# Kernel optimization log

Hardware: AMD Instinct MI355X
Metric: run time of the kernel (lower is better)

Reference implementation:

```python
import jax, jax.numpy as jnp
import numpy as np

R, N, C, E, H, NC = 25, 256, 64, 128, 8, 27


def _layernorm(x, w, b, axes, eps):
    m = x.mean(axis=axes, keepdims=True)
    v = x.var(axis=axes, keepdims=True)
    return (x - m) / jnp.sqrt(v + eps) * w + b


def _mha(emb_ln, idx, WQ, WK):
    # emb_ln: (R*N, E); idx: (L,) district indices
    ew = emb_ln.reshape(R, N, E)[idx]                       # (L,N,E) gather of district blocks
    Q = jnp.einsum('lne,hfe->lhnf', ew, WQ)                 # torch Linear: x @ W.T
    K = jnp.einsum('lne,hfe->lhnf', ew, WK)
    QK = jnp.einsum('lhnf,lhmf->lhnm', Q, K) / jnp.sqrt(jnp.float32(E))
    return jax.nn.softmax(QK, axis=2)                       # torch softmax(dim=1) over (L,n,n)


def setup_inputs() -> dict:
    key = jax.random.key(0)
    ks = jax.random.split(key, 16)
    inp = {
        'business_structure_target': jax.random.normal(ks[0], (R, C, N, 4), jnp.float32),
        'business_structure_infected': jax.random.normal(ks[1], (R, C, N, 4), jnp.float32),
        'customer_structure_target': jax.random.normal(ks[2], (R, C, N, NC, 4), jnp.float32),
        'customer_structure_infected': jax.random.normal(ks[3], (R, C, N, NC, 4), jnp.float32),
        'index_target_idx': jax.random.randint(ks[4], (R, C), 0, R),
        'index_infected_idx': jax.random.randint(ks[5], (R, C), 0, R),
        'covid_outbreak_business': jax.random.randint(ks[6], (R, C), 0, N),
        'emb_table': jax.random.normal(ks[7], (R * N, E), jnp.float32),
        'ln_emb_w': jnp.ones((E,), jnp.float32),
        'ln_emb_b': jnp.zeros((E,), jnp.float32),
        'WQ_trg': jax.random.normal(ks[8], (H, E, E), jnp.float32) * 0.05,
        'WK_trg': jax.random.normal(ks[9], (H, E, E), jnp.float32) * 0.05,
        'WQ_inf': jax.random.normal(ks[10], (H, E, E), jnp.float32) * 0.05,
        'WK_inf': jax.random.normal(ks[11], (H, E, E), jnp.float32) * 0.05,
        'W_os': jax.random.normal(ks[12], (E, E), jnp.float32) * 0.05,
        'b_os': jnp.zeros((E,), jnp.float32),
        'bs_w': jnp.ones((C, N), jnp.float32), 'bs_b': jnp.zeros((C, N), jnp.float32),
        'cs_w': jnp.ones((C, N), jnp.float32), 'cs_b': jnp.zeros((C, N), jnp.float32),
        'os_w': jnp.ones((C, N), jnp.float32), 'os_b': jnp.zeros((C, N), jnp.float32),
    }
    return inp


def reference(business_structure_target, business_structure_infected,
              customer_structure_target, customer_structure_infected,
              index_target_idx, index_infected_idx, covid_outbreak_business,
              emb_table, ln_emb_w, ln_emb_b,
              WQ_trg, WK_trg, WQ_inf, WK_inf,
              W_os, b_os, bs_w, bs_b, cs_w, cs_b, os_w, os_b):
    # mean over feature dim, then slicing per original forward
    bst = business_structure_target.mean(-1)[:R, 0]        # (R,N)
    bsi = business_structure_infected.mean(-1)[0]          # (C,N)
    cst = customer_structure_target.mean(-1)[:R, 0]        # (R,N,NC)
    csi = customer_structure_infected.mean(-1)[0]          # (C,N,NC)

    emb_ln = _layernorm(emb_table, ln_emb_w, ln_emb_b, -1, 1e-16)
    idx_t = index_target_idx[:R, 0]                        # (R,)
    idx_i = index_infected_idx[0]                          # (C,)

    attn_t = _mha(emb_ln, idx_t, WQ_trg, WK_trg)           # (R,H,N,N)
    BR_t = jnp.einsum('ln,lhnm->lmh', bst, attn_t)         # (R,N,H)
    attn_i = _mha(emb_ln, idx_i, WQ_inf, WK_inf)           # (C,H,N,N)
    BR_i = jnp.einsum('cn,chnm->cmh', bsi, attn_i)         # (C,N,H)

    # cosine similarity over head dim, broadcast (R,1,N,H) x (1,C,N,H)
    a = BR_t[:, None]
    b = BR_i[None]
    dot = jnp.sum(a * b, -1)
    na = jnp.linalg.norm(a, axis=-1)
    nb = jnp.linalg.norm(b, axis=-1)
    BS = dot / jnp.maximum(na * nb, 1e-15)                 # (R,C,N)

    # Jensen-Shannon-style KLD over consumer dim (log_target=True semantics)
    log_p = jax.nn.log_softmax(cst, -1)[:, None]           # (R,1,N,NC)
    log_q = jax.nn.log_softmax(csi, -1)[None]              # (1,C,N,NC)
    log_m = jax.nn.log_softmax((log_p + log_q) / 2, -1)
    kl_p = (jnp.exp(log_m) * (log_m - log_p)).mean(-1)
    kl_q = (jnp.exp(log_m) * (log_m - log_q)).mean(-1)
    CS = -(kl_p + kl_q) / 2                                # (R,C,N)

    biz = covid_outbreak_business[0]                       # (C,)
    inf_emb = emb_table[idx_i * N + biz]                   # (C,E) raw (non-LN) embedding
    proj = inf_emb @ W_os.T + b_os
    OS = (proj @ emb_table.T).reshape(C, R, N).transpose(1, 0, 2)  # (R,C,N)

    BS = _layernorm(BS, bs_w, bs_b, (-2, -1), 1e-5)
    CS = _layernorm(CS, cs_w, cs_b, (-2, -1), 1e-5)
    OS = _layernorm(OS, os_w, os_b, (-2, -1), 1e-5)
    return BS, CS, OS
```

## Files before the change

### kernel.cpp

```cpp
#include <hip/hip_runtime.h>
#include <math.h>

#define R_ 25
#define N_ 256
#define C_ 64
#define E_ 128
#define H_ 8
#define NC_ 27
#define SQS 28

typedef _Float16 f16x8 __attribute__((ext_vector_type(8)));
typedef float f32x16 __attribute__((ext_vector_type(16)));

union HU { ushort s; _Float16 h; };
__device__ __forceinline__ ushort ftoh(float f) { HU u; u.h = (_Float16)f; return u.s; }
__device__ __forceinline__ float htof(ushort s) { HU u; u.s = s; return (float)u.h; }

__device__ __forceinline__ float waveReduceSum(float v) {
  #pragma unroll
  for (int off = 32; off > 0; off >>= 1) v += __shfl_xor(v, off);
  return v;
}

__global__ __launch_bounds__(256) void k_prep(
    const float* __restrict__ emb, const float* __restrict__ ln_w,
    const float* __restrict__ ln_b, ushort* __restrict__ emb16,
    const float* __restrict__ bus_t, const float* __restrict__ bus_i,
    float* __restrict__ bst, float* __restrict__ bsi,
    const float* __restrict__ cus_t, const float* __restrict__ cus_i,
    float* __restrict__ Ssq, float* __restrict__ Tsq,
    const int* __restrict__ idx_t, const int* __restrict__ idx_i,
    int* __restrict__ cnt, int* __restrict__ lst,
    const int* __restrict__ biz, const float* __restrict__ Wos,
    const float* __restrict__ bos, float* __restrict__ projb,
    const float* __restrict__ WQt_, const float* __restrict__ WKt_,
    const float* __restrict__ WQi_, const float* __restrict__ WKi_,
    ushort* __restrict__ Gt) {
  __shared__ uint sbuf[16384];
  int bid = blockIdx.x, t = threadIdx.x;
  if (bid < 1600) {
    int row = bid * 4 + (t >> 6);
    int lane = t & 63;
    const float2* x = (const float2*)(emb + (size_t)row * E_);
    float2 v = x[lane];
    float s = waveReduceSum(v.x + v.y);
    float m = s * (1.0f / 128.0f);
    float d0 = v.x - m, d1 = v.y - m;
    float ss = waveReduceSum(d0 * d0 + d1 * d1);
    float inv = 1.0f / sqrtf(ss * (1.0f / 128.0f) + 1e-16f);
    float2 wv = ((const float2*)ln_w)[lane];
    float2 bv = ((const float2*)ln_b)[lane];
    uint u = (uint)ftoh(d0 * inv * wv.x + bv.x) | ((uint)ftoh(d1 * inv * wv.y + bv.y) << 16);
    ((uint*)emb16)[(size_t)row * 64 + lane] = u;
  } else if (bid < 1689) {
    int i = (bid - 1600) * 256 + t;
    if (i < R_ * N_) {
      size_t row = (size_t)(i >> 8) * (C_ * N_) + (i & 255);
      float4 v = *(const float4*)&bus_t[row * 4];
      bst[i] = (v.x + v.y + v.z + v.w) * 0.25f;
    }
    int j = i - R_ * N_;
    if (j >= 0 && j < C_ * N_) {
      float4 v = *(const float4*)&bus_i[(size_t)j * 4];
      bsi[j] = (v.x + v.y + v.z + v.w) * 0.25f;
    }
  } else if (bid < 2045) {
    int gidx = (bid - 1689) * 256 + t;
    int rowi = gidx >> 2, sub = gidx & 3;
    const float* src; float* dst; size_t base; int oi;
    if (rowi < R_ * N_) {
      src = cus_t; dst = Ssq; oi = rowi;
      base = ((size_t)(rowi >> 8) * (C_ * N_) + (rowi & 255)) * (NC_ * 4);
    } else {
      int j = rowi - R_ * N_;
      if (j >= C_ * N_) return;
      src = cus_i; dst = Tsq; oi = j;
      base = ((size_t)(j >> 8) * N_ + (j & 255)) * (NC_ * 4);
    }
    int j0 = sub * 7;
    int nj = (sub == 3) ? 6 : 7;
    float v[7];
    float mx = -1e30f;
    #pragma unroll
    for (int k = 0; k < 7; ++k) {
      if (k < nj) {
        float4 q = *(const float4*)&src[base + (j0 + k) * 4];
        v[k] = (q.x + q.y + q.z + q.w) * 0.25f;
        mx = fmaxf(mx, v[k]);
      }
    }
    mx = fmaxf(mx, __shfl_xor(mx, 1));
    mx = fmaxf(mx, __shfl_xor(mx, 2));
    float se = 0.0f;
    #pragma unroll
    for (int k = 0; k < 7; ++k) if (k < nj) se += expf(v[k] - mx);
    se += __shfl_xor(se, 1);
    se += __shfl_xor(se, 2);
    float lse = mx + logf(se);
    #pragma unroll
    for (int k = 0; k < 7; ++k)
      if (k < nj) dst[(size_t)oi * SQS + j0 + k] = expf(0.5f * (v[k] - lse));
    if (sub == 3) dst[(size_t)oi * SQS + NC_] = 0.0f;
  } else if (bid == 2045) {
    if (t < 2 * R_) cnt[t] = 0;
    __syncthreads();
    if (t < R_) {
      int rr = idx_t[t * C_];
      int pos = atomicAdd(&cnt[rr], 1);
      lst[rr * 64 + pos] = t;
    }
    if (t < C_) {
      int rr = idx_i[t];
      int pos = atomicAdd(&cnt[R_ + rr], 1);
      lst[(R_ + rr) * 64 + pos] = t;
    }
  } else if (bid < 2078) {
    float* er2 = (float*)sbuf;
    int pb = bid - 2046;
    int ci = t >> 7, f = t & 127;
    int c = pb * 2 + ci;
    int row = idx_i[c] * N_ + biz[c];
    er2[ci * E_ + f] = emb[(size_t)row * E_ + f];
    __syncthreads();
    float acc = bos[f];
    const float* wr = &Wos[(size_t)f * E_];
    const float* er = &er2[ci * E_];
    for (int e = 0; e < E_; e += 4) {
      float4 w4 = *(const float4*)&wr[e];
      acc += er[e] * w4.x + er[e + 1] * w4.y + er[e + 2] * w4.z + er[e + 3] * w4.w;
    }
    projb[c * E_ + f] = acc;
  } else {
    int gb = bid - 2078;
    int h = gb & 7, set = gb >> 3;
    const float* WQ = (set ? WQi_ : WQt_) + ((size_t)h << 14);
    const float* WK = (set ? WKi_ : WKt_) + ((size_t)h << 14);
    uint* QT = sbuf;
    uint* KT = sbuf + 8192;
    for (int j = t; j < 8192; j += 256) {
      int e = j & 127, f2 = j >> 7;
      int wi = (f2 << 8) + e;
      float q0 = WQ[wi], q1 = WQ[wi + 128];
      float k0 = WK[wi], k1 = WK[wi + 128];
      int idx = (e << 6) + (f2 ^ ((e & 15) << 2));
      QT[idx] = (uint)ftoh(q0) | ((uint)ftoh(q1) << 16);
      KT[idx] = (uint)ftoh(k0) | ((uint)ftoh(k1) << 16);
    }
    __syncthreads();
    int w = t >> 6, l = t & 63, lo = l & 31, hi = l >> 5;
    int m0 = w << 5;
    f32x16 acc[4];
    #pragma unroll
    for (int i = 0; i < 4; ++i)
      #pragma unroll
      for (int j = 0; j < 16; ++j) acc[i][j] = 0.0f;
    int mrow = m0 + lo;
    #pragma unroll
    for (int ks = 0; ks < 8; ++ks) {
      int f2b = (ks << 3) + (hi << 2);
      f16x8 a = *(const f16x8*)&KT[(mrow << 6) + (f2b ^ ((mrow & 15) << 2))];
      #pragma unroll
      for (int tl = 0; tl < 4; ++tl) {
        int ncol = (tl << 5) + lo;
        f16x8 b = *(const f16x8*)&QT[(ncol << 6) + (f2b ^ ((ncol & 15) << 2))];
        acc[tl] = __builtin_amdgcn_mfma_f32_32x32x16_f16(a, b, acc[tl], 0, 0, 0);
      }
    }
    const float scale = 0.08838834764831845f;
    ushort* Go = Gt + (((size_t)(set * H_ + h)) << 14);
    #pragma unroll
    for (int tl = 0; tl < 4; ++tl)
      #pragma unroll
      for (int rg = 0; rg < 16; ++rg) {
        int row = m0 + (rg & 3) + ((rg >> 2) << 3) + (hi << 2);
        int col = (tl << 5) + lo;
        Go[(row << 7) + col] = ftoh(acc[tl][rg] * scale);
      }
  }
}

__global__ __launch_bounds__(512) void k_attn_fused(
    const ushort* __restrict__ emb16, const ushort* __restrict__ GtAll,
    const int* __restrict__ cnt, const int* __restrict__ lst,
    const float* __restrict__ bst, const float* __restrict__ bsi,
    float* __restrict__ BRt, float* __restrict__ BRi) {
  int r = blockIdx.x, h = blockIdx.y, set = blockIdx.z;
  int g = set * R_ + r;
  int L = cnt[g];
  if (L == 0) return;
  __shared__ ushort ELN[256 * 128];
  __shared__ ushort TA[128 * 128];
  __shared__ ushort TB[128 * 128];
  __shared__ float redA[8 * 128];
  __shared__ float redB[8 * 128];
  __shared__ float gM[128], gD[128];
  int t = threadIdx.x;
  const uint4* Ep = (const uint4*)(emb16 + ((size_t)r << 15));
  for (int c = t; c < 4096; c += 512) {
    int n = c >> 4, s = c & 15;
    uint4 v = Ep[c];
    *(uint4*)&ELN[(n << 7) + ((s << 3) ^ ((n & 15) << 3))] = v;
  }
  const uint4* Gp = (const uint4*)(GtAll + ((size_t)(set * H_ + h) << 14));
  for (int c = t; c < 2048; c += 512) {
    int e2 = c >> 4, s = c & 15;
    uint4 v = Gp[c];
    *(uint4*)&TA[(e2 << 7) + ((s << 3) ^ ((e2 & 15) << 3))] = v;
  }
  __syncthreads();
  int w = t >> 6, l = t & 63, lo = l & 31, hi = l >> 5;
  f32x16 tacc[4];
  #pragma unroll
  for (int i = 0; i < 4; ++i)
    #pragma unroll
    for (int j = 0; j < 16; ++j) tacc[i][j] = 0.0f;
  int n = (w << 5) + lo;
  #pragma unroll
  for (int ks = 0; ks < 8; ++ks) {
    f16x8 a = *(const f16x8*)&ELN[(n << 7) + (((ks << 4) + (hi << 3)) ^ ((n & 15) << 3))];
    #pragma unroll
    for (int tl = 0; tl < 4; ++tl) {
      int f = (tl << 5) + lo;
      f16x8 b = *(const f16x8*)&TA[(f << 7) + (((ks << 4) + (hi << 3)) ^ ((f & 15) << 3))];
      tacc[tl] = __builtin_amdgcn_mfma_f32_32x32x16_f16(a, b, tacc[tl], 0, 0, 0);
    }
  }
  __syncthreads();
  {
    ushort* Tl = (w < 4) ? TA : TB;
    #pragma unroll
    for (int tl = 0; tl < 4; ++tl)
      #pragma unroll
      for (int rg = 0; rg < 16; ++rg) {
        int row = ((w & 3) << 5) + (rg & 3) + ((rg >> 2) << 3) + (hi << 2);
        int col = (tl << 5) + lo;
        Tl[(row << 7) + (col ^ ((row & 15) << 3))] = ftoh(tacc[tl][rg]);
      }
  }
  __syncthreads();
  const float* wv = set ? bsi : bst;
  float* BR = set ? BRi : BRt;
  const ushort* Tl = (w < 4) ? TA : TB;
  int rrow = n & 127;
  int baseRow = (w << 5) + (hi << 2);
  for (int mh = 0; mh < 2; ++mh) {
    f32x16 acc[4];
    #pragma unroll
    for (int i = 0; i < 4; ++i)
      #pragma unroll
      for (int j = 0; j < 16; ++j) acc[i][j] = 0.0f;
    #pragma unroll
    for (int ks = 0; ks < 8; ++ks) {
      f16x8 a = *(const f16x8*)&Tl[(rrow << 7) + (((ks << 4) + (hi << 3)) ^ ((rrow & 15) << 3))];
      #pragma unroll
      for (int tl = 0; tl < 4; ++tl) {
        int m = (mh << 7) + (tl << 5) + lo;
        f16x8 b = *(const f16x8*)&ELN[(m << 7) + (((ks << 4) + (hi << 3)) ^ ((m & 15) << 3))];
        acc[tl] = __builtin_amdgcn_mfma_f32_32x32x16_f16(a, b, acc[tl], 0, 0, 0);
      }
    }
    #pragma unroll
    for (int tl = 0; tl < 4; ++tl) {
      float mx = acc[tl][0];
      #pragma unroll
      for (int rg = 1; rg < 16; ++rg) mx = fmaxf(mx, acc[tl][rg]);
      mx = fmaxf(mx, __shfl_xor(mx, 32));
      if (hi == 0) redA[(w << 7) + (tl << 5) + lo] = mx;
    }
    __syncthreads();
    if (t < 128) {
      float gm = redA[t];
      #pragma unroll
      for (int ww = 1; ww < 8; ++ww) gm = fmaxf(gm, redA[(ww << 7) + t]);
      gM[t] = gm;
    }
    __syncthreads();
    #pragma unroll
    for (int tl = 0; tl < 4; ++tl) {
      float gmv = gM[(tl << 5) + lo];
      float s = 0.0f;
      #pragma unroll
      for (int rg = 0; rg < 16; ++rg) {
        acc[tl][rg] = __expf(acc[tl][rg] - gmv);
        s += acc[tl][rg];
      }
      s += __shfl_xor(s, 32);
      if (hi == 0) redB[(w << 7) + (tl << 5) + lo] = s;
    }
    __syncthreads();
    if (t < 128) {
      float d = 0.0f;
      #pragma unroll
      for (int ww = 0; ww < 8; ++ww) d += redB[(ww << 7) + t];
      gD[t] = d;
    }
    __syncthreads();
    for (int li = 0; li < L; ++li) {
      int ll = lst[g * 64 + li];
      float wreg[16];
      #pragma unroll
      for (int rg = 0; rg < 16; ++rg)
        wreg[rg] = wv[ll * N_ + baseRow + (rg & 3) + ((rg >> 2) << 3)];
      #pragma unroll
      for (int tl = 0; tl < 4; ++tl) {
        float part = 0.0f;
        #pragma unroll
        for (int rg = 0; rg < 16; ++rg) part += wreg[rg] * acc[tl][rg];
        part += __shfl_xor(part, 32);
        if (hi == 0) redA[(w << 7) + (tl << 5) + lo] = part;
      }
      __syncthreads();
      if (t < 128) {
        float s = 0.0f;
        #pragma unroll
        for (int ww = 0; ww < 8; ++ww) s += redA[(ww << 7) + t];
        BR[((size_t)ll * N_ + (mh << 7) + t) * H_ + h] = s / gD[t];
      }
      __syncthreads();
    }
  }
}

__global__ __launch_bounds__(256) void k_bscs_os(
    const float* __restrict__ BRt, const float* __restrict__ BRi,
    const float* __restrict__ Ssq, const float* __restrict__ Tsq,
    const float* __restrict__ emb, const float* __restrict__ projb,
    float* __restrict__ outBS, float* __restrict__ outCS,
    float* __restrict__ outOS,
    float2* __restrict__ pBS, float2* __restrict__ pCS,
    float2* __restrict__ pOS) {
  __shared__ float pr[8][E_];
  __shared__ float rb[4][4];
  int bid = blockIdx.x, t = threadIdx.x;
  if (bid < 1600) {
    int i = bid * 256 + t;
    int n = i & 255, c = (i >> 8) & 63, l = i >> 14;
    const float4* a = (const float4*)&BRt[((size_t)l * N_ + n) * H_];
    const float4* b = (const float4*)&BRi[((size_t)c * N_ + n) * H_];
    float4 a0 = a[0], a1 = a[1], b0 = b[0], b1 = b[1];
    float dot = a0.x * b0.x + a0.y * b0.y + a0.z * b0.z + a0.w * b0.w
              + a1.x * b1.x + a1.y * b1.y + a1.z * b1.z + a1.w * b1.w;
    float na = a0.x * a0.x + a0.y * a0.y + a0.z * a0.z + a0.w * a0.w
             + a1.x * a1.x + a1.y * a1.y + a1.z * a1.z + a1.w * a1.w;
    float nb = b0.x * b0.x + b0.y * b0.y + b0.z * b0.z + b0.w * b0.w
             + b1.x * b1.x + b1.y * b1.y + b1.z * b1.z + b1.w * b1.w;
    float bsv = dot / fmaxf(sqrtf(na) * sqrtf(nb), 1e-15f);
    outBS[i] = bsv;

    const float4* sp = (const float4*)&Ssq[((size_t)l * N_ + n) * SQS];
    const float4* tp = (const float4*)&Tsq[((size_t)c * N_ + n) * SQS];
    float d2 = 0.0f;
    #pragma unroll
    for (int j = 0; j < 7; ++j) {
      float4 sv = sp[j], tv = tp[j];
      d2 += sv.x * tv.x + sv.y * tv.y + sv.z * tv.z + sv.w * tv.w;
    }
    float csv = logf(d2) * (1.0f / 27.0f);
    outCS[i] = csv;
    float s0 = waveReduceSum(bsv), q0 = waveReduceSum(bsv * bsv);
    float s1 = waveReduceSum(csv), q1 = waveReduceSum(csv * csv);
    if ((t & 63) == 0) {
      int wv = t >> 6;
      rb[wv][0] = s0; rb[wv][1] = q0; rb[wv][2] = s1; rb[wv][3] = q1;
    }
    __syncthreads();
    if (t == 0) {
      float A = 0, B = 0, Cq = 0, D = 0;
      #pragma unroll
      for (int k = 0; k < 4; ++k) { A += rb[k][0]; B += rb[k][1]; Cq += rb[k][2]; D += rb[k][3]; }
      pBS[bid] = make_float2(A, B);
      pCS[bid] = make_float2(Cq, D);
    }
  } else {
    int o = bid - 1600;
    int l = o >> 3, cg = o & 7;
    for (int i = t; i < 1024; i += 256)
      pr[i >> 7][i & 127] = projb[(cg * 8 + (i >> 7)) * E_ + (i & 127)];
    __syncthreads();
    const float* er = &emb[((size_t)(l * N_) + t) << 7];
    float acc[8] = {0, 0, 0, 0, 0, 0, 0, 0};
    for (int e = 0; e < 128; e += 4) {
      float4 v = *(const float4*)&er[e];
      #pragma unroll
      for (int c = 0; c < 8; ++c)
        acc[c] += v.x * pr[c][e] + v.y * pr[c][e + 1] + v.z * pr[c][e + 2] + v.w * pr[c][e + 3];
    }
    float s = 0.0f, q = 0.0f;
    #pragma unroll
    for (int c = 0; c < 8; ++c) {
      outOS[((size_t)l * C_ + cg * 8 + c) * N_ + t] = acc[c];
      s += acc[c];
      q += acc[c] * acc[c];
    }
    s = waveReduceSum(s);
    q = waveReduceSum(q);
    if ((t & 63) == 0) { int wv = t >> 6; rb[wv][0] = s; rb[wv][1] = q; }
    __syncthreads();
    if (t == 0) {
      float A = 0, B = 0;
      #pragma unroll
      for (int k = 0; k < 4; ++k) { A += rb[k][0]; B += rb[k][1]; }
      pOS[o] = make_float2(A, B);
    }
  }
}

__global__ __launch_bounds__(256) void k_ln_apply(
    float* __restrict__ out,
    const float2* __restrict__ pBS, const float2* __restrict__ pCS,
    const float2* __restrict__ pOS,
    const float* __restrict__ w0, const float* __restrict__ b0,
    const float* __restrict__ w1, const float* __restrict__ b1,
    const float* __restrict__ w2, const float* __restrict__ b2) {
  int r = blockIdx.x, o = blockIdx.y, chunk = blockIdx.z;
  int t = threadIdx.x;
  __shared__ float sm[2];
  if (t < 64) {
    float s = 0.0f, q = 0.0f;
    if (o == 2) {
      if (t < 8) { float2 v = pOS[r * 8 + t]; s = v.x; q = v.y; }
    } else {
      const float2* pp = (o == 0) ? pBS : pCS;
      float2 v = pp[r * 64 + t]; s = v.x; q = v.y;
    }
    #pragma unroll
    for (int off = 32; off > 0; off >>= 1) {
      s += __shfl_xor(s, off);
      q += __shfl_xor(q, off);
    }
    if (t == 0) {
      float m = s * (1.0f / 16384.0f);
      float v = q * (1.0f / 16384.0f) - m * m;
      sm[0] = m;
      sm[1] = 1.0f / sqrtf(v + 1e-5f);
    }
  }
  __syncthreads();
  float m = sm[0], inv = sm[1];
  const float* w = (o == 0) ? w0 : (o == 1) ? w1 : w2;
  const float* b = (o == 0) ? b0 : (o == 1) ? b1 : b2;
  float* x = out + (size_t)o * 409600 + (size_t)r * 16384;
  int base = chunk * 2048;
  #pragma unroll
  for (int k = 0; k < 8; ++k) {
    int pos = base + k * 256 + t;
    x[pos] = (x[pos] - m) * inv * w[pos] + b[pos];
  }
}

extern "C" void kernel_launch(void* const* d_in, const int* in_sizes, int n_in,
                              void* d_out, int out_size, void* d_ws, size_t ws_size,
                              hipStream_t stream) {
  const float* bus_t  = (const float*)d_in[0];
  const float* bus_i  = (const float*)d_in[1];
  const float* cus_t  = (const float*)d_in[2];
  const float* cus_i  = (const float*)d_in[3];
  const int*   idx_t  = (const int*)d_in[4];
  const int*   idx_i  = (const int*)d_in[5];
  const int*   cov    = (const int*)d_in[6];
  const float* emb    = (const float*)d_in[7];
  const float* ln_w   = (const float*)d_in[8];
  const float* ln_b   = (const float*)d_in[9];
  const float* WQ_trg = (const float*)d_in[10];
  const float* WK_trg = (const float*)d_in[11];
  const float* WQ_inf = (const float*)d_in[12];
  const float* WK_inf = (const float*)d_in[13];
  const float* W_os   = (const float*)d_in[14];
  const float* b_os   = (const float*)d_in[15];
  const float* bs_w   = (const float*)d_in[16];
  const float* bs_b   = (const float*)d_in[17];
  const float* cs_w   = (const float*)d_in[18];
  const float* cs_b   = (const float*)d_in[19];
  const float* os_w   = (const float*)d_in[20];
  const float* os_b   = (const float*)d_in[21];

  float* ws = (float*)d_ws;
  ushort* emb16 = (ushort*)ws;
  float* p = ws + 409600;
  ushort* Gt = (ushort*)p;   p += 131072;
  float* bst = p;            p += 6400;
  float* bsi = p;            p += 16384;
  float* Ssq = p;            p += R_ * N_ * SQS;
  float* Tsq = p;            p += C_ * N_ * SQS;
  float* BRt = p;            p += 51200;
  float* BRi = p;            p += 131072;
  float* projb = p;          p += 8192;
  int* cnt = (int*)p;        p += 64;
  int* lst = (int*)p;        p += 3200;
  float2* pBS = (float2*)p;  p += 3200;
  float2* pCS = (float2*)p;  p += 3200;
  float2* pOS = (float2*)p;  p += 400;

  float* outBS = (float*)d_out;
  float* outCS = outBS + 409600;
  float* outOS = outCS + 409600;

  k_prep<<<2094, 256, 0, stream>>>(emb, ln_w, ln_b, emb16,
                                   bus_t, bus_i, bst, bsi,
                                   cus_t, cus_i, Ssq, Tsq,
                                   idx_t, idx_i, cnt, lst,
                                   cov, W_os, b_os, projb,
                                   WQ_trg, WK_trg, WQ_inf, WK_inf, Gt);
  k_attn_fused<<<dim3(R_, H_, 2), 512, 0, stream>>>(emb16, Gt, cnt, lst,
                                                    bst, bsi, BRt, BRi);
  k_bscs_os<<<1800, 256, 0, stream>>>(BRt, BRi, Ssq, Tsq, emb, projb,
                                      outBS, outCS, outOS, pBS, pCS, pOS);
  k_ln_apply<<<dim3(R_, 3, 8), 256, 0, stream>>>(outBS, pBS, pCS, pOS,
                                                 bs_w, bs_b, cs_w, cs_b, os_w, os_b);
}
```

Before: 84.56 us.

## Read attention operands from global memory and shrink LDS to raise occupancy

```diff
diff --git a/kernel.cpp b/kernel.cpp
--- a/kernel.cpp
+++ b/kernel.cpp
@@ -179,7 +179,7 @@
   }
 }
 
-__global__ __launch_bounds__(512) void k_attn_fused(
+__global__ __launch_bounds__(512, 4) void k_attn_fused(
     const ushort* __restrict__ emb16, const ushort* __restrict__ GtAll,
     const int* __restrict__ cnt, const int* __restrict__ lst,
     const float* __restrict__ bst, const float* __restrict__ bsi,
@@ -188,61 +188,46 @@
   int g = set * R_ + r;
   int L = cnt[g];
   if (L == 0) return;
-  __shared__ ushort ELN[256 * 128];
-  __shared__ ushort TA[128 * 128];
-  __shared__ ushort TB[128 * 128];
+  __shared__ ushort Tbuf[256 * 128];
   __shared__ float redA[8 * 128];
   __shared__ float redB[8 * 128];
   __shared__ float gM[128], gD[128];
   int t = threadIdx.x;
-  const uint4* Ep = (const uint4*)(emb16 + ((size_t)r << 15));
-  for (int c = t; c < 4096; c += 512) {
-    int n = c >> 4, s = c & 15;
-    uint4 v = Ep[c];
-    *(uint4*)&ELN[(n << 7) + ((s << 3) ^ ((n & 15) << 3))] = v;
-  }
-  const uint4* Gp = (const uint4*)(GtAll + ((size_t)(set * H_ + h) << 14));
-  for (int c = t; c < 2048; c += 512) {
-    int e2 = c >> 4, s = c & 15;
-    uint4 v = Gp[c];
-    *(uint4*)&TA[(e2 << 7) + ((s << 3) ^ ((e2 & 15) << 3))] = v;
-  }
-  __syncthreads();
   int w = t >> 6, l = t & 63, lo = l & 31, hi = l >> 5;
+  int n = (w << 5) + lo;
+  const ushort* Ebase = emb16 + ((size_t)r << 15);
+  const ushort* Gp = GtAll + ((size_t)(set * H_ + h) << 14);
+
   f32x16 tacc[4];
   #pragma unroll
   for (int i = 0; i < 4; ++i)
     #pragma unroll
     for (int j = 0; j < 16; ++j) tacc[i][j] = 0.0f;
-  int n = (w << 5) + lo;
+  {
+    const ushort* Ap = Ebase + ((size_t)n << 7) + (hi << 3);
+    #pragma unroll
+    for (int ks = 0; ks < 8; ++ks) {
+      f16x8 a = *(const f16x8*)(Ap + (ks << 4));
+      #pragma unroll
+      for (int tl = 0; tl < 4; ++tl) {
+        int f = (tl << 5) + lo;
+        f16x8 b = *(const f16x8*)(Gp + (f << 7) + (hi << 3) + (ks << 4));
+        tacc[tl] = __builtin_amdgcn_mfma_f32_32x32x16_f16(a, b, tacc[tl], 0, 0, 0);
+      }
+    }
+  }
   #pragma unroll
-  for (int ks = 0; ks < 8; ++ks) {
-    f16x8 a = *(const f16x8*)&ELN[(n << 7) + (((ks << 4) + (hi << 3)) ^ ((n & 15) << 3))];
-    #pragma unroll
-    for (int tl = 0; tl < 4; ++tl) {
-      int f = (tl << 5) + lo;
-      f16x8 b = *(const f16x8*)&TA[(f << 7) + (((ks << 4) + (hi << 3)) ^ ((f & 15) << 3))];
-      tacc[tl] = __builtin_amdgcn_mfma_f32_32x32x16_f16(a, b, tacc[tl], 0, 0, 0);
-    }
-  }
-  __syncthreads();
-  {
-    ushort* Tl = (w < 4) ? TA : TB;
-    #pragma unroll
-    for (int tl = 0; tl < 4; ++tl)
-      #pragma unroll
-      for (int rg = 0; rg < 16; ++rg) {
-        int row = ((w & 3) << 5) + (rg & 3) + ((rg >> 2) << 3) + (hi << 2);
-        int col = (tl << 5) + lo;
-        Tl[(row << 7) + (col ^ ((row & 15) << 3))] = ftoh(tacc[tl][rg]);
-      }
-  }
-  __syncthreads();
+  for (int tl = 0; tl < 4; ++tl)
+    #pragma unroll
+    for (int rg = 0; rg < 16; ++rg) {
+      int row = (w << 5) + (rg & 3) + ((rg >> 2) << 3) + (hi << 2);
+      int col = (tl << 5) + lo;
+      Tbuf[(row << 7) + (col ^ ((row & 15) << 3))] = ftoh(tacc[tl][rg]);
+    }
   const float* wv = set ? bsi : bst;
   float* BR = set ? BRi : BRt;
-  const ushort* Tl = (w < 4) ? TA : TB;
-  int rrow = n & 127;
   int baseRow = (w << 5) + (hi << 2);
+
   for (int mh = 0; mh < 2; ++mh) {
     f32x16 acc[4];
     #pragma unroll
@@ -251,11 +236,11 @@
       for (int j = 0; j < 16; ++j) acc[i][j] = 0.0f;
     #pragma unroll
     for (int ks = 0; ks < 8; ++ks) {
-      f16x8 a = *(const f16x8*)&Tl[(rrow << 7) + (((ks << 4) + (hi << 3)) ^ ((rrow & 15) << 3))];
+      f16x8 a = *(const f16x8*)&Tbuf[(n << 7) + (((ks << 4) + (hi << 3)) ^ ((n & 15) << 3))];
       #pragma unroll
       for (int tl = 0; tl < 4; ++tl) {
         int m = (mh << 7) + (tl << 5) + lo;
-        f16x8 b = *(const f16x8*)&ELN[(m << 7) + (((ks << 4) + (hi << 3)) ^ ((m & 15) << 3))];
+        f16x8 b = *(const f16x8*)(Ebase + ((size_t)m << 7) + (hi << 3) + (ks << 4));
         acc[tl] = __builtin_amdgcn_mfma_f32_32x32x16_f16(a, b, acc[tl], 0, 0, 0);
       }
     }
```

Measured after the change: 105.2 us. +24.4%, slower.

## Transpose attention score tile so softmax and weighted sums stay within each wave

Applied to the files above, without the earlier changes.

```diff
diff --git a/kernel.cpp b/kernel.cpp
--- a/kernel.cpp
+++ b/kernel.cpp
@@ -191,10 +191,9 @@
   __shared__ ushort ELN[256 * 128];
   __shared__ ushort TA[128 * 128];
   __shared__ ushort TB[128 * 128];
-  __shared__ float redA[8 * 128];
-  __shared__ float redB[8 * 128];
-  __shared__ float gM[128], gD[128];
   int t = threadIdx.x;
+  int w = t >> 6, l = t & 63, lo = l & 31, hi = l >> 5;
+
   const uint4* Ep = (const uint4*)(emb16 + ((size_t)r << 15));
   for (int c = t; c < 4096; c += 512) {
     int n = c >> 4, s = c & 15;
@@ -208,25 +207,25 @@
     *(uint4*)&TA[(e2 << 7) + ((s << 3) ^ ((e2 & 15) << 3))] = v;
   }
   __syncthreads();
-  int w = t >> 6, l = t & 63, lo = l & 31, hi = l >> 5;
-  f32x16 tacc[4];
-  #pragma unroll
-  for (int i = 0; i < 4; ++i)
-    #pragma unroll
-    for (int j = 0; j < 16; ++j) tacc[i][j] = 0.0f;
-  int n = (w << 5) + lo;
-  #pragma unroll
-  for (int ks = 0; ks < 8; ++ks) {
-    f16x8 a = *(const f16x8*)&ELN[(n << 7) + (((ks << 4) + (hi << 3)) ^ ((n & 15) << 3))];
-    #pragma unroll
-    for (int tl = 0; tl < 4; ++tl) {
-      int f = (tl << 5) + lo;
-      f16x8 b = *(const f16x8*)&TA[(f << 7) + (((ks << 4) + (hi << 3)) ^ ((f & 15) << 3))];
-      tacc[tl] = __builtin_amdgcn_mfma_f32_32x32x16_f16(a, b, tacc[tl], 0, 0, 0);
-    }
-  }
-  __syncthreads();
+
   {
+    f32x16 tacc[4];
+    #pragma unroll
+    for (int i = 0; i < 4; ++i)
+      #pragma unroll
+      for (int j = 0; j < 16; ++j) tacc[i][j] = 0.0f;
+    int n = (w << 5) + lo;
+    #pragma unroll
+    for (int ks = 0; ks < 8; ++ks) {
+      f16x8 a = *(const f16x8*)&ELN[(n << 7) + (((ks << 4) + (hi << 3)) ^ ((n & 15) << 3))];
+      #pragma unroll
+      for (int tl = 0; tl < 4; ++tl) {
+        int f = (tl << 5) + lo;
+        f16x8 b = *(const f16x8*)&TA[(f << 7) + (((ks << 4) + (hi << 3)) ^ ((f & 15) << 3))];
+        tacc[tl] = __builtin_amdgcn_mfma_f32_32x32x16_f16(a, b, tacc[tl], 0, 0, 0);
+      }
+    }
+    __syncthreads();
     ushort* Tl = (w < 4) ? TA : TB;
     #pragma unroll
     for (int tl = 0; tl < 4; ++tl)
@@ -238,85 +237,65 @@
       }
   }
   __syncthreads();
+
+  f32x16 acc[8];
+  #pragma unroll
+  for (int i = 0; i < 8; ++i)
+    #pragma unroll
+    for (int j = 0; j < 16; ++j) acc[i][j] = 0.0f;
+  {
+    int m = (w << 5) + lo;
+    #pragma unroll
+    for (int ks = 0; ks < 8; ++ks) {
+      f16x8 a = *(const f16x8*)&ELN[(m << 7) + (((ks << 4) + (hi << 3)) ^ ((m & 15) << 3))];
+      #pragma unroll
+      for (int tl = 0; tl < 8; ++tl) {
+        int nn = ((tl & 3) << 5) + lo;
+        const ushort* Tl = (tl < 4) ? TA : TB;
+        f16x8 b = *(const f16x8*)&Tl[(nn << 7) + (((ks << 4) + (hi << 3)) ^ ((nn & 15) << 3))];
+        acc[tl] = __builtin_amdgcn_mfma_f32_32x32x16_f16(a, b, acc[tl], 0, 0, 0);
+      }
+    }
+  }
+
+  float den[16];
+  #pragma unroll
+  for (int rg = 0; rg < 16; ++rg) {
+    float mx = acc[0][rg];
+    #pragma unroll
+    for (int tl = 1; tl < 8; ++tl) mx = fmaxf(mx, acc[tl][rg]);
+    #pragma unroll
+    for (int off = 16; off > 0; off >>= 1) mx = fmaxf(mx, __shfl_xor(mx, off));
+    float s = 0.0f;
+    #pragma unroll
+    for (int tl = 0; tl < 8; ++tl) {
+      acc[tl][rg] = __expf(acc[tl][rg] - mx);
+      s += acc[tl][rg];
+    }
+    #pragma unroll
+    for (int off = 16; off > 0; off >>= 1) s += __shfl_xor(s, off);
+    den[rg] = s;
+  }
+
   const float* wv = set ? bsi : bst;
   float* BR = set ? BRi : BRt;
-  const ushort* Tl = (w < 4) ? TA : TB;
-  int rrow = n & 127;
-  int baseRow = (w << 5) + (hi << 2);
-  for (int mh = 0; mh < 2; ++mh) {
-    f32x16 acc[4];
-    #pragma unroll
-    for (int i = 0; i < 4; ++i)
-      #pragma unroll
-      for (int j = 0; j < 16; ++j) acc[i][j] = 0.0f;
-    #pragma unroll
-    for (int ks = 0; ks < 8; ++ks) {
-      f16x8 a = *(const f16x8*)&Tl[(rrow << 7) + (((ks << 4) + (hi << 3)) ^ ((rrow & 15) << 3))];
-      #pragma unroll
-      for (int tl = 0; tl < 4; ++tl) {
-        int m = (mh << 7) + (tl << 5) + lo;
-        f16x8 b = *(const f16x8*)&ELN[(m << 7) + (((ks << 4) + (hi << 3)) ^ ((m & 15) << 3))];
-        acc[tl] = __builtin_amdgcn_mfma_f32_32x32x16_f16(a, b, acc[tl], 0, 0, 0);
-      }
-    }
-    #pragma unroll
-    for (int tl = 0; tl < 4; ++tl) {
-      float mx = acc[tl][0];
-      #pragma unroll
-      for (int rg = 1; rg < 16; ++rg) mx = fmaxf(mx, acc[tl][rg]);
-      mx = fmaxf(mx, __shfl_xor(mx, 32));
-      if (hi == 0) redA[(w << 7) + (tl << 5) + lo] = mx;
-    }
-    __syncthreads();
-    if (t < 128) {
-      float gm = redA[t];
-      #pragma unroll
-      for (int ww = 1; ww < 8; ++ww) gm = fmaxf(gm, redA[(ww << 7) + t]);
-      gM[t] = gm;
-    }
-    __syncthreads();
-    #pragma unroll
-    for (int tl = 0; tl < 4; ++tl) {
-      float gmv = gM[(tl << 5) + lo];
-      float s = 0.0f;
-      #pragma unroll
-      for (int rg = 0; rg < 16; ++rg) {
-        acc[tl][rg] = __expf(acc[tl][rg] - gmv);
-        s += acc[tl][rg];
-      }
-      s += __shfl_xor(s, 32);
-      if (hi == 0) redB[(w << 7) + (tl << 5) + lo] = s;
-    }
-    __syncthreads();
-    if (t < 128) {
-      float d = 0.0f;
-      #pragma unroll
-      for (int ww = 0; ww < 8; ++ww) d += redB[(ww << 7) + t];
-      gD[t] = d;
-    }
-    __syncthreads();
-    for (int li = 0; li < L; ++li) {
-      int ll = lst[g * 64 + li];
-      float wreg[16];
-      #pragma unroll
-      for (int rg = 0; rg < 16; ++rg)
-        wreg[rg] = wv[ll * N_ + baseRow + (rg & 3) + ((rg >> 2) << 3)];
-      #pragma unroll
-      for (int tl = 0; tl < 4; ++tl) {
-        float part = 0.0f;
-        #pragma unroll
-        for (int rg = 0; rg < 16; ++rg) part += wreg[rg] * acc[tl][rg];
-        part += __shfl_xor(part, 32);
-        if (hi == 0) redA[(w << 7) + (tl << 5) + lo] = part;
-      }
-      __syncthreads();
-      if (t < 128) {
-        float s = 0.0f;
-        #pragma unroll
-        for (int ww = 0; ww < 8; ++ww) s += redA[(ww << 7) + t];
-        BR[((size_t)ll * N_ + (mh << 7) + t) * H_ + h] = s / gD[t];
-      }
-      __syncthreads();
+  for (int li = 0; li < L; ++li) {
+    int ll = lst[g * 64 + li];
+    const float* wr = wv + (size_t)ll * N_;
+    float bw[8];
+    #pragma unroll
+    for (int tl = 0; tl < 8; ++tl) bw[tl] = wr[(tl << 5) + lo];
+    #pragma unroll
+    for (int rg = 0; rg < 16; ++rg) {
+      float p = 0.0f;
+      #pragma unroll
+      for (int tl = 0; tl < 8; ++tl) p += bw[tl] * acc[tl][rg];
+      #pragma unroll
+      for (int off = 16; off > 0; off >>= 1) p += __shfl_xor(p, off);
+      if (lo == 0) {
+        int m = (w << 5) + (rg & 3) + ((rg >> 2) << 3) + (hi << 2);
+        BR[((size_t)ll * N_ + m) * H_ + h] = p / den[rg];
+      }
     }
   }
 }
```

Result: slower. 98.26 us (+16.2%).
